# Kernel optimization log

Measured on AMD Instinct MI355X. Metric: run time of the kernel, lower is better.

## Reference

```python
import jax, jax.numpy as jnp
import numpy as np

HEADS = 8
MODEL_DIM = 64
EPS = 1e-5


def _layernorm(x, gamma, beta):
    mu = jnp.mean(x, axis=-1, keepdims=True)
    var = jnp.var(x, axis=-1, keepdims=True)
    return (x - mu) * jax.lax.rsqrt(var + EPS) * gamma + beta


def setup_inputs() -> dict:
    key = jax.random.key(0)
    ks = jax.random.split(key, 5)
    bs, h, w, in_dim = 8, 32, 32, 512
    hd = HEADS * MODEL_DIM  # 512
    s = 0.02
    return {
        "x": jax.random.normal(ks[0], (bs, h, w, in_dim), jnp.float32),
        "Wq": jax.random.normal(ks[1], (in_dim, hd), jnp.float32) * s,
        "Wk": jax.random.normal(ks[2], (in_dim, hd), jnp.float32) * s,
        "Wv": jax.random.normal(ks[3], (in_dim, hd), jnp.float32) * s,
        "Wo": jax.random.normal(ks[4], (hd, in_dim), jnp.float32) * s,
        "gamma": jnp.ones((in_dim,), jnp.float32),
        "beta": jnp.zeros((in_dim,), jnp.float32),
    }


def reference(x, Wq, Wk, Wv, Wo, gamma, beta):
    bs, h, w, in_dim = x.shape
    # pre_norm=True: normalize first; residual uses the normalized x (as in original)
    xn = _layernorm(x, gamma, beta)
    Q = (xn @ Wq).reshape(bs, h, w, HEADS, MODEL_DIM)
    K = (xn @ Wk).reshape(bs, h, w, HEADS, MODEL_DIM)
    V = (xn @ Wv).reshape(bs, h, w, HEADS, MODEL_DIM)
    # full (h,w) x (h,w) correlation per head
    corr = jnp.einsum('bijhd,bklhd->bijhkl', Q, K) / jnp.sqrt(
        jnp.asarray(MODEL_DIM, x.dtype))
    cshape = corr.shape
    attn = jax.nn.softmax(corr.reshape(*cshape[:-2], -1), axis=-1).reshape(cshape)
    logits = jnp.einsum('bijhkl,bklhd->bijhd', attn, V).reshape(bs, h, w, -1)
    out = logits @ Wo + xn
    return out, attn
```

## Files before the change

### kernel.cpp

```cpp
#include <hip/hip_runtime.h>
#include <hip/hip_bf16.h>

typedef __attribute__((ext_vector_type(8))) short bf16x8;
typedef __attribute__((ext_vector_type(4))) short s16x4;
typedef __attribute__((ext_vector_type(4))) float f32x4;

#define DIM 512
#define NH 8
#define HD 64
#define SEQ 1024
#define NB 8
#define ROWS (NB*SEQ)

__device__ __forceinline__ short f2bf(float f) {
  union { float f; unsigned u; } v; v.f = f;
  unsigned r = v.u + 0x7fffu + ((v.u >> 16) & 1u);
  return (short)(r >> 16);
}
__device__ __forceinline__ float bf2f(short s) {
  union { unsigned u; float f; } v; v.u = ((unsigned)(unsigned short)s) << 16;
  return v.f;
}
__device__ __forceinline__ f32x4 mfma16(bf16x8 a, bf16x8 b, f32x4 c) {
  return __builtin_amdgcn_mfma_f32_16x16x32_bf16(a, b, c, 0, 0, 0);
}
__device__ __forceinline__ void gload16(const void* g, void* l) {
  __builtin_amdgcn_global_load_lds(
      (const __attribute__((address_space(1))) unsigned int*)g,
      (__attribute__((address_space(3))) unsigned int*)l, 16, 0, 0);
}
__device__ __forceinline__ void lds_barrier() {
  __builtin_amdgcn_sched_barrier(0);
  asm volatile("s_waitcnt lgkmcnt(0)" ::: "memory");
  __builtin_amdgcn_s_barrier();
  __builtin_amdgcn_sched_barrier(0);
}

__global__ __launch_bounds__(256) void prep_kernel(
    const float* __restrict__ x, const float* __restrict__ gamma,
    const float* __restrict__ beta, short* __restrict__ xnb,
    const float* __restrict__ Wq, const float* __restrict__ Wk,
    const float* __restrict__ Wv, const float* __restrict__ Wo,
    short* __restrict__ WqkvT, short* __restrict__ WoT) {
  __shared__ float tl[64 * 65];
  const int t = threadIdx.x;
  if (blockIdx.x < 2048) {
    const int row = blockIdx.x * 4 + (t >> 6);
    const int lane = t & 63;
    const float4* xr = reinterpret_cast<const float4*>(x + (size_t)row * DIM);
    const float4 a = xr[lane * 2], b2 = xr[lane * 2 + 1];
    float s = a.x + a.y + a.z + a.w + b2.x + b2.y + b2.z + b2.w;
    float sq = a.x*a.x + a.y*a.y + a.z*a.z + a.w*a.w +
               b2.x*b2.x + b2.y*b2.y + b2.z*b2.z + b2.w*b2.w;
    for (int off = 1; off < 64; off <<= 1) {
      s += __shfl_xor(s, off);
      sq += __shfl_xor(sq, off);
    }
    const float mean = s * (1.0f / DIM);
    const float var = sq * (1.0f / DIM) - mean * mean;
    const float rs = rsqrtf(var + 1e-5f);
    const float4 ga = reinterpret_cast<const float4*>(gamma)[lane * 2];
    const float4 gb = reinterpret_cast<const float4*>(gamma)[lane * 2 + 1];
    const float4 ba = reinterpret_cast<const float4*>(beta)[lane * 2];
    const float4 bb = reinterpret_cast<const float4*>(beta)[lane * 2 + 1];
    union { bf16x8 v; short sh[8]; } o;
    o.sh[0] = f2bf((a.x - mean) * rs * ga.x + ba.x);
    o.sh[1] = f2bf((a.y - mean) * rs * ga.y + ba.y);
    o.sh[2] = f2bf((a.z - mean) * rs * ga.z + ba.z);
    o.sh[3] = f2bf((a.w - mean) * rs * ga.w + ba.w);
    o.sh[4] = f2bf((b2.x - mean) * rs * gb.x + bb.x);
    o.sh[5] = f2bf((b2.y - mean) * rs * gb.y + bb.y);
    o.sh[6] = f2bf((b2.z - mean) * rs * gb.z + bb.z);
    o.sh[7] = f2bf((b2.w - mean) * rs * gb.w + bb.w);
    *reinterpret_cast<bf16x8*>(xnb + (size_t)row * DIM + lane * 8) = o.v;
  } else {
    const int bb = blockIdx.x - 2048;
    const int y = bb >> 6;
    const float* W = (y == 0) ? Wq : (y == 1) ? Wk : (y == 2) ? Wv : Wo;
    const int tile = bb & 63;
    const int k0 = (tile >> 3) * 64, n0 = (tile & 7) * 64;
#pragma unroll
    for (int i = 0; i < 16; ++i) {
      const int idx = i * 256 + t;
      const int k = idx >> 6, n = idx & 63;
      tl[n * 65 + k] = W[(size_t)(k0 + k) * 512 + n0 + n];
    }
    __syncthreads();
#pragma unroll
    for (int i = 0; i < 16; ++i) {
      const int idx = i * 256 + t;
      const int n = idx >> 6, k = idx & 63;
      const short v = f2bf(tl[n * 65 + k]);
      if (y < 3) WqkvT[(size_t)(y * 512 + n0 + n) * 512 + k0 + k] = v;
      else       WoT[(size_t)(n0 + n) * 512 + k0 + k] = v;
    }
  }
}

#define GEMM64_MAIN(A_, BT_, m0_, n0_)                                        \
  f32x4 acc[4][4] = {};                                                       \
  {                                                                           \
    const int srow = 8 * w + (lane >> 3);                                     \
    const int sseg = lane & 7;                                                \
    for (int kb = 0; kb < 512; kb += 64) {                                    \
      __syncthreads();                                                        \
      _Pragma("unroll")                                                       \
      for (int p = 0; p < 4; ++p) {                                           \
        const int r = 32 * p + srow;                                          \
        const int gs = 8 * (sseg ^ (r & 7));                                  \
        gload16(A_ + (size_t)(m0_ + r) * 512 + kb + gs,                       \
                &As[(32 * p + 8 * w) * 64]);                                  \
        gload16(BT_ + (size_t)(n0_ + r) * 512 + kb + gs,                      \
                &Bs[(32 * p + 8 * w) * 64]);                                  \
      }                                                                       \
      __syncthreads();                                                        \
      _Pragma("unroll")                                                       \
      for (int half = 0; half < 2; ++half) {                                  \
        bf16x8 af[4], bfr[4];                                                 \
        _Pragma("unroll")                                                     \
        for (int i = 0; i < 4; ++i) {                                         \
          const int ra = 64 * wr + 16 * i + c16;                              \
          af[i] = *reinterpret_cast<const bf16x8*>(                           \
              &As[ra * 64 + 8 * ((4 * half + g) ^ (ra & 7))]);                \
          const int rb = 64 * wc + 16 * i + c16;                              \
          bfr[i] = *reinterpret_cast<const bf16x8*>(                          \
              &Bs[rb * 64 + 8 * ((4 * half + g) ^ (rb & 7))]);                \
        }                                                                     \
        _Pragma("unroll")                                                     \
        for (int i = 0; i < 4; ++i)                                           \
          _Pragma("unroll")                                                   \
          for (int j = 0; j < 4; ++j)                                         \
            acc[i][j] = mfma16(af[i], bfr[j], acc[i][j]);                     \
      }                                                                       \
    }                                                                         \
  }

__global__ __launch_bounds__(256) void gemm_qkv(const short* __restrict__ A,
    const short* __restrict__ BT, short* __restrict__ Qo,
    short* __restrict__ Ko, short* __restrict__ VtF) {
  __shared__ short As[128 * 64];
  __shared__ short Bs[128 * 64];
  const int m0 = blockIdx.x * 128, n0 = blockIdx.y * 128;
  const int t = threadIdx.x, w = t >> 6, lane = t & 63, g = lane >> 4, c16 = lane & 15;
  const int wr = w >> 1, wc = w & 1;
  GEMM64_MAIN(A, BT, m0, n0)
  const int z = n0 >> 9;
  const int nl = n0 & 511;
  if (z < 2) {
    short* O = (z == 0) ? Qo : Ko;
#pragma unroll
    for (int i = 0; i < 4; ++i)
#pragma unroll
      for (int j = 0; j < 4; ++j) {
        const int row0 = m0 + 64 * wr + 16 * i + 4 * g;
        const int col = nl + 64 * wc + 16 * j + c16;
#pragma unroll
        for (int e = 0; e < 4; ++e)
          O[(size_t)(row0 + e) * 512 + col] = f2bf(acc[i][j][e]);
      }
  } else {
#pragma unroll
    for (int i = 0; i < 4; ++i)
#pragma unroll
      for (int j = 0; j < 4; ++j) {
        const int row0 = m0 + 64 * wr + 16 * i + 4 * g;
        const int col = nl + 64 * wc + 16 * j + c16;
        const int bb = row0 >> 10, ss0 = row0 & 1023, hh = col >> 6, dd = col & 63;
        const int cch = ss0 >> 7, kk = ss0 & 127;
        const int w2 = kk >> 5;
        const int g2 = (kk >> 2) & 3;
        const int ee0 = 4 * ((kk >> 4) & 1) + (kk & 3);
        const int dt2 = dd >> 4, c162 = dd & 15;
        s16x4 pv;
#pragma unroll
        for (int e = 0; e < 4; ++e) pv[e] = f2bf(acc[i][j][e]);
        *reinterpret_cast<s16x4*>(
            &VtF[((size_t)((((bb * NH + hh) * 8 + cch) * 4 + w2) * 4 + dt2) << 9) +
                 (g2 * 16 + c162) * 8 + ee0]) = pv;
      }
  }
}

__global__ __launch_bounds__(256) void gemm_out(const short* __restrict__ A,
    const short* __restrict__ BT, const short* __restrict__ xnb,
    float* __restrict__ out) {
  __shared__ short As[128 * 64];
  __shared__ short Bs[128 * 64];
  const int m0 = blockIdx.x * 128, n0 = blockIdx.y * 128;
  const int t = threadIdx.x, w = t >> 6, lane = t & 63, g = lane >> 4, c16 = lane & 15;
  const int wr = w >> 1, wc = w & 1;
  GEMM64_MAIN(A, BT, m0, n0)
#pragma unroll
  for (int i = 0; i < 4; ++i)
#pragma unroll
    for (int j = 0; j < 4; ++j)
#pragma unroll
      for (int e = 0; e < 4; ++e) {
        const int row = m0 + 64 * wr + 16 * i + 4 * g + e;
        const int col = n0 + 64 * wc + 16 * j + c16;
        const size_t idx = (size_t)row * 512 + col;
        out[idx] = acc[i][j][e] + bf2f(xnb[idx]);
      }
}

__global__ __launch_bounds__(256, 2) void attn_kernel(
    const short* __restrict__ Qb, const short* __restrict__ Kb,
    const short* __restrict__ VtF, float* __restrict__ attnOut,
    short* __restrict__ Lg) {
  const int bid = blockIdx.x;
  const int rb = (bid >> 3) & 31;
  const int inst = (bid & 7) * 8 + (bid >> 8);
  const int b = inst >> 3, h = inst & 7;
  const int t = threadIdx.x;
  const int w = t >> 6, lane = t & 63, g = lane >> 4, c16 = lane & 15;
  const int rl = lane >> 3, sgl = lane & 7;

  __shared__ __align__(16) char smem[49664];
  __shared__ float red[2][4][16];
  short* Klds = (short*)smem;
  float* P32a = (float*)(smem + 32768);
  float* P32b = (float*)(smem + 41216);

  const short* qpa = Qb + ((size_t)(b * SEQ + rb * 32 + c16)) * DIM + h * HD + 8 * g;
  const bf16x8 qa0 = *reinterpret_cast<const bf16x8*>(qpa);
  const bf16x8 qa1 = *reinterpret_cast<const bf16x8*>(qpa + 32);
  const bf16x8 qB0 = *reinterpret_cast<const bf16x8*>(qpa + 16 * DIM);
  const bf16x8 qB1 = *reinterpret_cast<const bf16x8*>(qpa + 16 * DIM + 32);

  const short* kgbase = Kb + ((size_t)b * SEQ) * DIM + h * HD;
  const int swz = 8 * (sgl ^ rl);
  const int sw = c16 & 7;

#define KSTAGE(c_, buf_)                                                       \
  do {                                                                         \
    __builtin_amdgcn_sched_barrier(0);                                         \
    _Pragma("unroll") for (int i_ = 0; i_ < 4; ++i_) {                         \
      gload16(kgbase + (size_t)((c_) * 128 + 32 * w + 8 * i_ + rl) * DIM + swz,\
              &Klds[(buf_) * 8192 + (32 * w + 8 * i_) * 64]);                  \
    }                                                                          \
  } while (0)

  KSTAGE(0, 0);
  f32x4 acc[16] = {};
#pragma unroll
  for (int c = 0; c < 8; ++c) {
    if (c < 7) KSTAGE(c + 1, (c + 1) & 1);
    if (c < 7) { asm volatile("s_waitcnt vmcnt(4)" ::: "memory"); }
    else       { asm volatile("s_waitcnt vmcnt(0)" ::: "memory"); }
    __builtin_amdgcn_sched_barrier(0);
    const short* kl = &Klds[(c & 1) * 8192];
#pragma unroll
    for (int j = 0; j < 2; ++j) {
      const int lr = 32 * w + 16 * j + c16;
      bf16x8 k0 = *reinterpret_cast<const bf16x8*>(&kl[lr * 64 + 8 * (g ^ sw)]);
      bf16x8 k1 = *reinterpret_cast<const bf16x8*>(&kl[lr * 64 + 8 * ((g + 4) ^ sw)]);
      const int tt = c * 2 + j;
      acc[tt] = mfma16(k0, qa0, acc[tt]);
      acc[tt] = mfma16(k1, qa1, acc[tt]);
    }
  }

  const short* vf = VtF + (size_t)inst * 65536;
  bf16x8 vreg[4];
#pragma unroll
  for (int dt = 0; dt < 4; ++dt)
    vreg[dt] = *reinterpret_cast<const bf16x8*>(vf + (size_t)((w * 4 + dt) * 512) + lane * 8);
  bf16x8 kreg[4];
#pragma unroll
  for (int i = 0; i < 4; ++i)
    kreg[i] = *reinterpret_cast<const bf16x8*>(
        kgbase + (size_t)(32 * w + 8 * i + rl) * DIM + 8 * sgl);

  float m = -1e30f;
#pragma unroll
  for (int tt = 0; tt < 16; ++tt)
#pragma unroll
    for (int e = 0; e < 4; ++e) {
      acc[tt][e] *= 0.125f;
      m = fmaxf(m, acc[tt][e]);
    }
  m = fmaxf(m, __shfl_xor(m, 16));
  m = fmaxf(m, __shfl_xor(m, 32));
  if (g == 0) red[0][w][c16] = m;
  lds_barrier();
  m = fmaxf(fmaxf(red[0][0][c16], red[0][1][c16]),
            fmaxf(red[0][2][c16], red[0][3][c16]));
  float sm = 0.f;
#pragma unroll
  for (int tt = 0; tt < 16; ++tt)
#pragma unroll
    for (int e = 0; e < 4; ++e) {
      const float p = __expf(acc[tt][e] - m);
      acc[tt][e] = p;
      sm += p;
    }
  sm += __shfl_xor(sm, 16);
  sm += __shfl_xor(sm, 32);
  if (g == 0) red[1][w][c16] = sm;
  lds_barrier();
  const float rinvA = 1.0f / (red[1][0][c16] + red[1][1][c16] +
                              red[1][2][c16] + red[1][3][c16]);

  bf16x8 pA[8];
#pragma unroll
  for (int c = 0; c < 8; ++c) {
    union { bf16x8 v; short sh[8]; } u;
#pragma unroll
    for (int j = 0; j < 2; ++j)
#pragma unroll
      for (int e = 0; e < 4; ++e)
        u.sh[4 * j + e] = f2bf(acc[2 * c + j][e] * rinvA);
    pA[c] = u.v;
  }
#pragma unroll
  for (int tt = 0; tt < 16; ++tt)
#pragma unroll
    for (int e = 0; e < 4; ++e) acc[tt][e] = 0.f;

  f32x4 paccA[4] = {};
  const int qrow = t >> 4, qs = t & 15;
  float* astore = attnOut + (size_t)b * 8388608 +
                  (size_t)(rb * 32 + qrow) * 8192 + h * 1024;
#pragma unroll
  for (int c = 0; c < 8; ++c) {
    lds_barrier();
#pragma unroll
    for (int i = 0; i < 4; ++i)
      *reinterpret_cast<bf16x8*>(
          &Klds[(c & 1) * 8192 + (32 * w + 8 * i + rl) * 64 + 8 * (sgl ^ rl)]) = kreg[i];
    {
      float* P32w = (c & 1) ? P32b : P32a;
      union { bf16x8 v; short sh[8]; } u; u.v = pA[c];
      f32x4 v0, v1;
#pragma unroll
      for (int e = 0; e < 4; ++e) { v0[e] = bf2f(u.sh[e]); v1[e] = bf2f(u.sh[4 + e]); }
      *reinterpret_cast<f32x4*>(&P32w[c16 * 132 + 32 * w + 4 * g]) = v0;
      *reinterpret_cast<f32x4*>(&P32w[c16 * 132 + 32 * w + 16 + 4 * g]) = v1;
    }
    if (c < 7) {
#pragma unroll
      for (int i = 0; i < 4; ++i)
        kreg[i] = *reinterpret_cast<const bf16x8*>(
            kgbase + (size_t)((c + 1) * 128 + 32 * w + 8 * i + rl) * DIM + 8 * sgl);
    }
    lds_barrier();
    {
      const float* P32r = (c & 1) ? P32b : P32a;
      const f32x4 s0 = *reinterpret_cast<const f32x4*>(&P32r[qrow * 132 + 4 * qs]);
      const f32x4 s1 = *reinterpret_cast<const f32x4*>(&P32r[qrow * 132 + 64 + 4 * qs]);
      *reinterpret_cast<f32x4*>(astore + c * 128 + 4 * qs) = s0;
      *reinterpret_cast<f32x4*>(astore + c * 128 + 64 + 4 * qs) = s1;
    }
    const short* kl = &Klds[(c & 1) * 8192];
#pragma unroll
    for (int j = 0; j < 2; ++j) {
      const int lr = 32 * w + 16 * j + c16;
      bf16x8 k0 = *reinterpret_cast<const bf16x8*>(&kl[lr * 64 + 8 * (g ^ sw)]);
      bf16x8 k1 = *reinterpret_cast<const bf16x8*>(&kl[lr * 64 + 8 * ((g + 4) ^ sw)]);
      const int tt = c * 2 + j;
      acc[tt] = mfma16(k0, qB0, acc[tt]);
      acc[tt] = mfma16(k1, qB1, acc[tt]);
    }
#pragma unroll
    for (int dt = 0; dt < 4; ++dt)
      paccA[dt] = mfma16(pA[c], vreg[dt], paccA[dt]);
    if (c < 7) {
#pragma unroll
      for (int dt = 0; dt < 4; ++dt)
        vreg[dt] = *reinterpret_cast<const bf16x8*>(
            vf + (size_t)((((c + 1) * 4 + w) * 4 + dt) * 512) + lane * 8);
    }
  }

#pragma unroll
  for (int dt = 0; dt < 4; ++dt)
    vreg[dt] = *reinterpret_cast<const bf16x8*>(vf + (size_t)((w * 4 + dt) * 512) + lane * 8);

  float mB = -1e30f;
#pragma unroll
  for (int tt = 0; tt < 16; ++tt)
#pragma unroll
    for (int e = 0; e < 4; ++e) {
      acc[tt][e] *= 0.125f;
      mB = fmaxf(mB, acc[tt][e]);
    }
  mB = fmaxf(mB, __shfl_xor(mB, 16));
  mB = fmaxf(mB, __shfl_xor(mB, 32));
  if (g == 0) red[0][w][c16] = mB;
  lds_barrier();
  mB = fmaxf(fmaxf(red[0][0][c16], red[0][1][c16]),
             fmaxf(red[0][2][c16], red[0][3][c16]));
  float smB = 0.f;
#pragma unroll
  for (int tt = 0; tt < 16; ++tt)
#pragma unroll
    for (int e = 0; e < 4; ++e) {
      const float p = __expf(acc[tt][e] - mB);
      acc[tt][e] = p;
      smB += p;
    }
  smB += __shfl_xor(smB, 16);
  smB += __shfl_xor(smB, 32);
  if (g == 0) red[1][w][c16] = smB;
  lds_barrier();
  const float rinvB = 1.0f / (red[1][0][c16] + red[1][1][c16] +
                              red[1][2][c16] + red[1][3][c16]);
  bf16x8 pB[8];
#pragma unroll
  for (int c = 0; c < 8; ++c) {
    union { bf16x8 v; short sh[8]; } u;
#pragma unroll
    for (int j = 0; j < 2; ++j)
#pragma unroll
      for (int e = 0; e < 4; ++e)
        u.sh[4 * j + e] = f2bf(acc[2 * c + j][e] * rinvB);
    pB[c] = u.v;
  }

  f32x4 paccB[4] = {};
  float* astoreB = astore + 16 * 8192;
#pragma unroll
  for (int c = 0; c < 8; ++c) {
    lds_barrier();
    {
      float* P32w = (c & 1) ? P32b : P32a;
      union { bf16x8 v; short sh[8]; } u; u.v = pB[c];
      f32x4 v0, v1;
#pragma unroll
      for (int e = 0; e < 4; ++e) { v0[e] = bf2f(u.sh[e]); v1[e] = bf2f(u.sh[4 + e]); }
      *reinterpret_cast<f32x4*>(&P32w[c16 * 132 + 32 * w + 4 * g]) = v0;
      *reinterpret_cast<f32x4*>(&P32w[c16 * 132 + 32 * w + 16 + 4 * g]) = v1;
    }
    lds_barrier();
    {
      const float* P32r = (c & 1) ? P32b : P32a;
      const f32x4 s0 = *reinterpret_cast<const f32x4*>(&P32r[qrow * 132 + 4 * qs]);
      const f32x4 s1 = *reinterpret_cast<const f32x4*>(&P32r[qrow * 132 + 64 + 4 * qs]);
      *reinterpret_cast<f32x4*>(astoreB + c * 128 + 4 * qs) = s0;
      *reinterpret_cast<f32x4*>(astoreB + c * 128 + 64 + 4 * qs) = s1;
    }
#pragma unroll
    for (int dt = 0; dt < 4; ++dt)
      paccB[dt] = mfma16(pB[c], vreg[dt], paccB[dt]);
    if (c < 7) {
#pragma unroll
      for (int dt = 0; dt < 4; ++dt)
        vreg[dt] = *reinterpret_cast<const bf16x8*>(
            vf + (size_t)((((c + 1) * 4 + w) * 4 + dt) * 512) + lane * 8);
    }
  }

  lds_barrier();
  f32x4* red2 = reinterpret_cast<f32x4*>(smem);
#pragma unroll
  for (int dt = 0; dt < 4; ++dt) red2[(w * 4 + dt) * 64 + lane] = paccA[dt];
  lds_barrier();
  {
    const int dt = w;
    f32x4 s = red2[dt * 64 + lane];
#pragma unroll
    for (int w2 = 1; w2 < 4; ++w2) {
      f32x4 o = red2[(w2 * 4 + dt) * 64 + lane];
#pragma unroll
      for (int e = 0; e < 4; ++e) s[e] += o[e];
    }
    short* lrow = Lg + ((size_t)(b * SEQ + rb * 32 + 4 * g)) * DIM + h * HD + 16 * dt + c16;
#pragma unroll
    for (int e = 0; e < 4; ++e) lrow[(size_t)e * DIM] = f2bf(s[e]);
  }
  lds_barrier();
#pragma unroll
  for (int dt = 0; dt < 4; ++dt) red2[(w * 4 + dt) * 64 + lane] = paccB[dt];
  lds_barrier();
  {
    const int dt = w;
    f32x4 s = red2[dt * 64 + lane];
#pragma unroll
    for (int w2 = 1; w2 < 4; ++w2) {
      f32x4 o = red2[(w2 * 4 + dt) * 64 + lane];
#pragma unroll
      for (int e = 0; e < 4; ++e) s[e] += o[e];
    }
    short* lrow = Lg + ((size_t)(b * SEQ + rb * 32 + 16 + 4 * g)) * DIM + h * HD + 16 * dt + c16;
#pragma unroll
    for (int e = 0; e < 4; ++e) lrow[(size_t)e * DIM] = f2bf(s[e]);
  }
}

extern "C" void kernel_launch(void* const* d_in, const int* in_sizes, int n_in,
                              void* d_out, int out_size, void* d_ws, size_t ws_size,
                              hipStream_t stream) {
  const float* x = (const float*)d_in[0];
  const float* Wq = (const float*)d_in[1];
  const float* Wk = (const float*)d_in[2];
  const float* Wv = (const float*)d_in[3];
  const float* Wo = (const float*)d_in[4];
  const float* gamma = (const float*)d_in[5];
  const float* beta = (const float*)d_in[6];
  float* out = (float*)d_out;
  float* attn = out + (size_t)ROWS * DIM;

  char* ws = (char*)d_ws;
  short* xnb = (short*)ws;
  short* WqkvT = (short*)(ws + (size_t)8 * 1024 * 1024);
  short* WoT = WqkvT + 1536 * 512;
  short* Qb = (short*)(ws + (size_t)10 * 1024 * 1024);
  short* Kbp = (short*)(ws + (size_t)18 * 1024 * 1024);
  short* VtF = (short*)(ws + (size_t)26 * 1024 * 1024);
  short* Lg = (short*)(ws + (size_t)34 * 1024 * 1024);

  prep_kernel<<<2304, 256, 0, stream>>>(x, gamma, beta, xnb, Wq, Wk, Wv, Wo, WqkvT, WoT);
  gemm_qkv<<<dim3(64, 12), 256, 0, stream>>>(xnb, WqkvT, Qb, Kbp, VtF);
  attn_kernel<<<2048, 256, 0, stream>>>(Qb, Kbp, VtF, attn, Lg);
  gemm_out<<<dim3(64, 4), 256, 0, stream>>>(Lg, WoT, xnb, out);
}
```

Measured before the change: 128.4 us.

## Process 64 query rows per block with a rolling software pipeline over four tiles

Each attention block now handles four 16-row query tiles instead of two. It halves the grid and overlaps the QK^T MFMA of the next tile with the attention store and PV MFMA of the current tile in a steady-state loop. K and V are reloaded cyclically across tiles, and each tile's output reduction is folded into the softmax barriers. Attention-probability stores become nontemporal. This is meant to amortise K/V staging and overlap compute with the large attn write, at the cost of fewer blocks (lower parallelism and occupancy slack) and more complex barrier use.

```diff
diff --git a/kernel.cpp b/kernel.cpp
--- a/kernel.cpp
+++ b/kernel.cpp
@@ -208,12 +208,15 @@
     const short* __restrict__ VtF, float* __restrict__ attnOut,
     short* __restrict__ Lg) {
   const int bid = blockIdx.x;
-  const int rb = (bid >> 3) & 31;
-  const int inst = (bid & 7) * 8 + (bid >> 8);
+  const int rb = (bid >> 3) & 15;
+  const int inst = (bid & 7) * 8 + (bid >> 7);
   const int b = inst >> 3, h = inst & 7;
   const int t = threadIdx.x;
   const int w = t >> 6, lane = t & 63, g = lane >> 4, c16 = lane & 15;
   const int rl = lane >> 3, sgl = lane & 7;
+  const int sw = c16 & 7;
+  const int rbase = rb * 64;
+  const int qrow = t >> 4, qs = t & 15;
 
   __shared__ __align__(16) char smem[49664];
   __shared__ float red[2][4][16];
@@ -221,15 +224,9 @@
   float* P32a = (float*)(smem + 32768);
   float* P32b = (float*)(smem + 41216);
 
-  const short* qpa = Qb + ((size_t)(b * SEQ + rb * 32 + c16)) * DIM + h * HD + 8 * g;
-  const bf16x8 qa0 = *reinterpret_cast<const bf16x8*>(qpa);
-  const bf16x8 qa1 = *reinterpret_cast<const bf16x8*>(qpa + 32);
-  const bf16x8 qB0 = *reinterpret_cast<const bf16x8*>(qpa + 16 * DIM);
-  const bf16x8 qB1 = *reinterpret_cast<const bf16x8*>(qpa + 16 * DIM + 32);
-
   const short* kgbase = Kb + ((size_t)b * SEQ) * DIM + h * HD;
+  const short* vf = VtF + (size_t)inst * 65536;
   const int swz = 8 * (sgl ^ rl);
-  const int sw = c16 & 7;
 
 #define KSTAGE(c_, buf_)                                                       \
   do {                                                                         \
@@ -240,250 +237,235 @@
     }                                                                          \
   } while (0)
 
-  KSTAGE(0, 0);
   f32x4 acc[16] = {};
-#pragma unroll
-  for (int c = 0; c < 8; ++c) {
-    if (c < 7) KSTAGE(c + 1, (c + 1) & 1);
-    if (c < 7) { asm volatile("s_waitcnt vmcnt(4)" ::: "memory"); }
-    else       { asm volatile("s_waitcnt vmcnt(0)" ::: "memory"); }
-    __builtin_amdgcn_sched_barrier(0);
-    const short* kl = &Klds[(c & 1) * 8192];
-#pragma unroll
-    for (int j = 0; j < 2; ++j) {
-      const int lr = 32 * w + 16 * j + c16;
-      bf16x8 k0 = *reinterpret_cast<const bf16x8*>(&kl[lr * 64 + 8 * (g ^ sw)]);
-      bf16x8 k1 = *reinterpret_cast<const bf16x8*>(&kl[lr * 64 + 8 * ((g + 4) ^ sw)]);
-      const int tt = c * 2 + j;
-      acc[tt] = mfma16(k0, qa0, acc[tt]);
-      acc[tt] = mfma16(k1, qa1, acc[tt]);
-    }
-  }
-
-  const short* vf = VtF + (size_t)inst * 65536;
-  bf16x8 vreg[4];
-#pragma unroll
-  for (int dt = 0; dt < 4; ++dt)
-    vreg[dt] = *reinterpret_cast<const bf16x8*>(vf + (size_t)((w * 4 + dt) * 512) + lane * 8);
-  bf16x8 kreg[4];
+  {
+    const short* qp = Qb + ((size_t)(b * SEQ + rbase + c16)) * DIM + h * HD + 8 * g;
+    const bf16x8 q0 = *reinterpret_cast<const bf16x8*>(qp);
+    const bf16x8 q1 = *reinterpret_cast<const bf16x8*>(qp + 32);
+    KSTAGE(0, 0);
+#pragma unroll
+    for (int c = 0; c < 8; ++c) {
+      if (c < 7) KSTAGE(c + 1, (c + 1) & 1);
+      if (c < 7) { asm volatile("s_waitcnt vmcnt(4)" ::: "memory"); }
+      else       { asm volatile("s_waitcnt vmcnt(0)" ::: "memory"); }
+      __builtin_amdgcn_sched_barrier(0);
+      const short* kl = &Klds[(c & 1) * 8192];
+#pragma unroll
+      for (int j = 0; j < 2; ++j) {
+        const int lr = 32 * w + 16 * j + c16;
+        bf16x8 k0 = *reinterpret_cast<const bf16x8*>(&kl[lr * 64 + 8 * (g ^ sw)]);
+        bf16x8 k1 = *reinterpret_cast<const bf16x8*>(&kl[lr * 64 + 8 * ((g + 4) ^ sw)]);
+        const int tt = c * 2 + j;
+        acc[tt] = mfma16(k0, q0, acc[tt]);
+        acc[tt] = mfma16(k1, q1, acc[tt]);
+      }
+    }
+  }
+
+  bf16x8 kreg[4], vreg[4];
 #pragma unroll
   for (int i = 0; i < 4; ++i)
     kreg[i] = *reinterpret_cast<const bf16x8*>(
         kgbase + (size_t)(32 * w + 8 * i + rl) * DIM + 8 * sgl);
-
-  float m = -1e30f;
-#pragma unroll
-  for (int tt = 0; tt < 16; ++tt)
-#pragma unroll
-    for (int e = 0; e < 4; ++e) {
-      acc[tt][e] *= 0.125f;
-      m = fmaxf(m, acc[tt][e]);
-    }
-  m = fmaxf(m, __shfl_xor(m, 16));
-  m = fmaxf(m, __shfl_xor(m, 32));
-  if (g == 0) red[0][w][c16] = m;
-  lds_barrier();
-  m = fmaxf(fmaxf(red[0][0][c16], red[0][1][c16]),
-            fmaxf(red[0][2][c16], red[0][3][c16]));
-  float sm = 0.f;
-#pragma unroll
-  for (int tt = 0; tt < 16; ++tt)
-#pragma unroll
-    for (int e = 0; e < 4; ++e) {
-      const float p = __expf(acc[tt][e] - m);
-      acc[tt][e] = p;
-      sm += p;
-    }
-  sm += __shfl_xor(sm, 16);
-  sm += __shfl_xor(sm, 32);
-  if (g == 0) red[1][w][c16] = sm;
-  lds_barrier();
-  const float rinvA = 1.0f / (red[1][0][c16] + red[1][1][c16] +
-                              red[1][2][c16] + red[1][3][c16]);
-
-  bf16x8 pA[8];
-#pragma unroll
-  for (int c = 0; c < 8; ++c) {
-    union { bf16x8 v; short sh[8]; } u;
-#pragma unroll
-    for (int j = 0; j < 2; ++j)
-#pragma unroll
-      for (int e = 0; e < 4; ++e)
-        u.sh[4 * j + e] = f2bf(acc[2 * c + j][e] * rinvA);
-    pA[c] = u.v;
-  }
-#pragma unroll
-  for (int tt = 0; tt < 16; ++tt)
-#pragma unroll
-    for (int e = 0; e < 4; ++e) acc[tt][e] = 0.f;
-
-  f32x4 paccA[4] = {};
-  const int qrow = t >> 4, qs = t & 15;
-  float* astore = attnOut + (size_t)b * 8388608 +
-                  (size_t)(rb * 32 + qrow) * 8192 + h * 1024;
-#pragma unroll
-  for (int c = 0; c < 8; ++c) {
-    lds_barrier();
-#pragma unroll
-    for (int i = 0; i < 4; ++i)
-      *reinterpret_cast<bf16x8*>(
-          &Klds[(c & 1) * 8192 + (32 * w + 8 * i + rl) * 64 + 8 * (sgl ^ rl)]) = kreg[i];
-    {
-      float* P32w = (c & 1) ? P32b : P32a;
-      union { bf16x8 v; short sh[8]; } u; u.v = pA[c];
-      f32x4 v0, v1;
-#pragma unroll
-      for (int e = 0; e < 4; ++e) { v0[e] = bf2f(u.sh[e]); v1[e] = bf2f(u.sh[4 + e]); }
-      *reinterpret_cast<f32x4*>(&P32w[c16 * 132 + 32 * w + 4 * g]) = v0;
-      *reinterpret_cast<f32x4*>(&P32w[c16 * 132 + 32 * w + 16 + 4 * g]) = v1;
-    }
-    if (c < 7) {
-#pragma unroll
-      for (int i = 0; i < 4; ++i)
-        kreg[i] = *reinterpret_cast<const bf16x8*>(
-            kgbase + (size_t)((c + 1) * 128 + 32 * w + 8 * i + rl) * DIM + 8 * sgl);
-    }
-    lds_barrier();
-    {
-      const float* P32r = (c & 1) ? P32b : P32a;
-      const f32x4 s0 = *reinterpret_cast<const f32x4*>(&P32r[qrow * 132 + 4 * qs]);
-      const f32x4 s1 = *reinterpret_cast<const f32x4*>(&P32r[qrow * 132 + 64 + 4 * qs]);
-      *reinterpret_cast<f32x4*>(astore + c * 128 + 4 * qs) = s0;
-      *reinterpret_cast<f32x4*>(astore + c * 128 + 64 + 4 * qs) = s1;
-    }
-    const short* kl = &Klds[(c & 1) * 8192];
-#pragma unroll
-    for (int j = 0; j < 2; ++j) {
-      const int lr = 32 * w + 16 * j + c16;
-      bf16x8 k0 = *reinterpret_cast<const bf16x8*>(&kl[lr * 64 + 8 * (g ^ sw)]);
-      bf16x8 k1 = *reinterpret_cast<const bf16x8*>(&kl[lr * 64 + 8 * ((g + 4) ^ sw)]);
-      const int tt = c * 2 + j;
-      acc[tt] = mfma16(k0, qB0, acc[tt]);
-      acc[tt] = mfma16(k1, qB1, acc[tt]);
-    }
-#pragma unroll
-    for (int dt = 0; dt < 4; ++dt)
-      paccA[dt] = mfma16(pA[c], vreg[dt], paccA[dt]);
-    if (c < 7) {
-#pragma unroll
-      for (int dt = 0; dt < 4; ++dt)
-        vreg[dt] = *reinterpret_cast<const bf16x8*>(
-            vf + (size_t)((((c + 1) * 4 + w) * 4 + dt) * 512) + lane * 8);
-    }
-  }
-
 #pragma unroll
   for (int dt = 0; dt < 4; ++dt)
     vreg[dt] = *reinterpret_cast<const bf16x8*>(vf + (size_t)((w * 4 + dt) * 512) + lane * 8);
 
-  float mB = -1e30f;
-#pragma unroll
-  for (int tt = 0; tt < 16; ++tt)
-#pragma unroll
-    for (int e = 0; e < 4; ++e) {
-      acc[tt][e] *= 0.125f;
-      mB = fmaxf(mB, acc[tt][e]);
-    }
-  mB = fmaxf(mB, __shfl_xor(mB, 16));
-  mB = fmaxf(mB, __shfl_xor(mB, 32));
-  if (g == 0) red[0][w][c16] = mB;
-  lds_barrier();
-  mB = fmaxf(fmaxf(red[0][0][c16], red[0][1][c16]),
-             fmaxf(red[0][2][c16], red[0][3][c16]));
-  float smB = 0.f;
-#pragma unroll
-  for (int tt = 0; tt < 16; ++tt)
-#pragma unroll
-    for (int e = 0; e < 4; ++e) {
-      const float p = __expf(acc[tt][e] - mB);
-      acc[tt][e] = p;
-      smB += p;
-    }
-  smB += __shfl_xor(smB, 16);
-  smB += __shfl_xor(smB, 32);
-  if (g == 0) red[1][w][c16] = smB;
-  lds_barrier();
-  const float rinvB = 1.0f / (red[1][0][c16] + red[1][1][c16] +
-                              red[1][2][c16] + red[1][3][c16]);
-  bf16x8 pB[8];
-#pragma unroll
-  for (int c = 0; c < 8; ++c) {
-    union { bf16x8 v; short sh[8]; } u;
-#pragma unroll
-    for (int j = 0; j < 2; ++j)
-#pragma unroll
-      for (int e = 0; e < 4; ++e)
-        u.sh[4 * j + e] = f2bf(acc[2 * c + j][e] * rinvB);
-    pB[c] = u.v;
-  }
-
-  f32x4 paccB[4] = {};
-  float* astoreB = astore + 16 * 8192;
-#pragma unroll
-  for (int c = 0; c < 8; ++c) {
+  bf16x8 pA[8];
+  {
+    float m = -1e30f;
+#pragma unroll
+    for (int tt = 0; tt < 16; ++tt)
+#pragma unroll
+      for (int e = 0; e < 4; ++e) {
+        acc[tt][e] *= 0.125f;
+        m = fmaxf(m, acc[tt][e]);
+      }
+    m = fmaxf(m, __shfl_xor(m, 16));
+    m = fmaxf(m, __shfl_xor(m, 32));
+    if (g == 0) red[0][w][c16] = m;
     lds_barrier();
-    {
-      float* P32w = (c & 1) ? P32b : P32a;
-      union { bf16x8 v; short sh[8]; } u; u.v = pB[c];
-      f32x4 v0, v1;
-#pragma unroll
-      for (int e = 0; e < 4; ++e) { v0[e] = bf2f(u.sh[e]); v1[e] = bf2f(u.sh[4 + e]); }
-      *reinterpret_cast<f32x4*>(&P32w[c16 * 132 + 32 * w + 4 * g]) = v0;
-      *reinterpret_cast<f32x4*>(&P32w[c16 * 132 + 32 * w + 16 + 4 * g]) = v1;
-    }
+    m = fmaxf(fmaxf(red[0][0][c16], red[0][1][c16]),
+              fmaxf(red[0][2][c16], red[0][3][c16]));
+    float sm = 0.f;
+#pragma unroll
+    for (int tt = 0; tt < 16; ++tt)
+#pragma unroll
+      for (int e = 0; e < 4; ++e) {
+        const float p = __expf(acc[tt][e] - m);
+        acc[tt][e] = p;
+        sm += p;
+      }
+    sm += __shfl_xor(sm, 16);
+    sm += __shfl_xor(sm, 32);
+    if (g == 0) red[1][w][c16] = sm;
     lds_barrier();
-    {
-      const float* P32r = (c & 1) ? P32b : P32a;
-      const f32x4 s0 = *reinterpret_cast<const f32x4*>(&P32r[qrow * 132 + 4 * qs]);
-      const f32x4 s1 = *reinterpret_cast<const f32x4*>(&P32r[qrow * 132 + 64 + 4 * qs]);
-      *reinterpret_cast<f32x4*>(astoreB + c * 128 + 4 * qs) = s0;
-      *reinterpret_cast<f32x4*>(astoreB + c * 128 + 64 + 4 * qs) = s1;
-    }
-#pragma unroll
-    for (int dt = 0; dt < 4; ++dt)
-      paccB[dt] = mfma16(pB[c], vreg[dt], paccB[dt]);
-    if (c < 7) {
+    const float rinv = 1.0f / (red[1][0][c16] + red[1][1][c16] +
+                               red[1][2][c16] + red[1][3][c16]);
+#pragma unroll
+    for (int c = 0; c < 8; ++c) {
+      union { bf16x8 v; short sh[8]; } u;
+#pragma unroll
+      for (int j = 0; j < 2; ++j)
+#pragma unroll
+        for (int e = 0; e < 4; ++e) {
+          u.sh[4 * j + e] = f2bf(acc[2 * c + j][e] * rinv);
+          acc[2 * c + j][e] = 0.f;
+        }
+      pA[c] = u.v;
+    }
+  }
+
+  f32x4 pacc[4] = {};
+  f32x4* red2 = reinterpret_cast<f32x4*>(smem + 32768);
+
+#pragma unroll
+  for (int tau = 0; tau < 4; ++tau) {
+    const bool qk = (tau < 3);
+    bf16x8 qn0, qn1;
+    if (qk) {
+      const short* qn = Qb + ((size_t)(b * SEQ + rbase + (tau + 1) * 16 + c16)) * DIM +
+                        h * HD + 8 * g;
+      qn0 = *reinterpret_cast<const bf16x8*>(qn);
+      qn1 = *reinterpret_cast<const bf16x8*>(qn + 32);
+    }
+    float* astore = attnOut + (size_t)b * 8388608 +
+                    (size_t)(rbase + tau * 16 + qrow) * 8192 + h * 1024;
+#pragma unroll
+    for (int c = 0; c < 8; ++c) {
+      lds_barrier();
+      if (qk) {
+#pragma unroll
+        for (int i = 0; i < 4; ++i)
+          *reinterpret_cast<bf16x8*>(
+              &Klds[(c & 1) * 8192 + (32 * w + 8 * i + rl) * 64 + 8 * (sgl ^ rl)]) = kreg[i];
+      }
+      {
+        float* P32w = (c & 1) ? P32b : P32a;
+        union { bf16x8 v; short sh[8]; } u; u.v = pA[c];
+        f32x4 v0, v1;
+#pragma unroll
+        for (int e = 0; e < 4; ++e) { v0[e] = bf2f(u.sh[e]); v1[e] = bf2f(u.sh[4 + e]); }
+        *reinterpret_cast<f32x4*>(&P32w[c16 * 132 + 32 * w + 4 * g]) = v0;
+        *reinterpret_cast<f32x4*>(&P32w[c16 * 132 + 32 * w + 16 + 4 * g]) = v1;
+      }
+      if (qk) {
+#pragma unroll
+        for (int i = 0; i < 4; ++i)
+          kreg[i] = *reinterpret_cast<const bf16x8*>(
+              kgbase + (size_t)((((c + 1) & 7)) * 128 + 32 * w + 8 * i + rl) * DIM + 8 * sgl);
+      }
+      lds_barrier();
+      {
+        const float* P32r = (c & 1) ? P32b : P32a;
+        const f32x4 s0 = *reinterpret_cast<const f32x4*>(&P32r[qrow * 132 + 4 * qs]);
+        const f32x4 s1 = *reinterpret_cast<const f32x4*>(&P32r[qrow * 132 + 64 + 4 * qs]);
+        __builtin_nontemporal_store(s0, reinterpret_cast<f32x4*>(astore + c * 128 + 4 * qs));
+        __builtin_nontemporal_store(s1, reinterpret_cast<f32x4*>(astore + c * 128 + 64 + 4 * qs));
+      }
+      if (qk) {
+        const short* kl = &Klds[(c & 1) * 8192];
+#pragma unroll
+        for (int j = 0; j < 2; ++j) {
+          const int lr = 32 * w + 16 * j + c16;
+          bf16x8 k0 = *reinterpret_cast<const bf16x8*>(&kl[lr * 64 + 8 * (g ^ sw)]);
+          bf16x8 k1 = *reinterpret_cast<const bf16x8*>(&kl[lr * 64 + 8 * ((g + 4) ^ sw)]);
+          const int tt = c * 2 + j;
+          acc[tt] = mfma16(k0, qn0, acc[tt]);
+          acc[tt] = mfma16(k1, qn1, acc[tt]);
+        }
+      }
 #pragma unroll
       for (int dt = 0; dt < 4; ++dt)
-        vreg[dt] = *reinterpret_cast<const bf16x8*>(
-            vf + (size_t)((((c + 1) * 4 + w) * 4 + dt) * 512) + lane * 8);
-    }
-  }
-
-  lds_barrier();
-  f32x4* red2 = reinterpret_cast<f32x4*>(smem);
-#pragma unroll
-  for (int dt = 0; dt < 4; ++dt) red2[(w * 4 + dt) * 64 + lane] = paccA[dt];
-  lds_barrier();
-  {
-    const int dt = w;
-    f32x4 s = red2[dt * 64 + lane];
-#pragma unroll
-    for (int w2 = 1; w2 < 4; ++w2) {
-      f32x4 o = red2[(w2 * 4 + dt) * 64 + lane];
-#pragma unroll
-      for (int e = 0; e < 4; ++e) s[e] += o[e];
-    }
-    short* lrow = Lg + ((size_t)(b * SEQ + rb * 32 + 4 * g)) * DIM + h * HD + 16 * dt + c16;
-#pragma unroll
-    for (int e = 0; e < 4; ++e) lrow[(size_t)e * DIM] = f2bf(s[e]);
-  }
-  lds_barrier();
-#pragma unroll
-  for (int dt = 0; dt < 4; ++dt) red2[(w * 4 + dt) * 64 + lane] = paccB[dt];
-  lds_barrier();
-  {
-    const int dt = w;
-    f32x4 s = red2[dt * 64 + lane];
-#pragma unroll
-    for (int w2 = 1; w2 < 4; ++w2) {
-      f32x4 o = red2[(w2 * 4 + dt) * 64 + lane];
-#pragma unroll
-      for (int e = 0; e < 4; ++e) s[e] += o[e];
-    }
-    short* lrow = Lg + ((size_t)(b * SEQ + rb * 32 + 16 + 4 * g)) * DIM + h * HD + 16 * dt + c16;
-#pragma unroll
-    for (int e = 0; e < 4; ++e) lrow[(size_t)e * DIM] = f2bf(s[e]);
+        pacc[dt] = mfma16(pA[c], vreg[dt], pacc[dt]);
+      if (!(tau == 3 && c == 7)) {
+#pragma unroll
+        for (int dt = 0; dt < 4; ++dt)
+          vreg[dt] = *reinterpret_cast<const bf16x8*>(
+              vf + (size_t)(((((c + 1) & 7) * 4 + w) * 4 + dt) * 512) + lane * 8);
+      }
+    }
+
+    if (qk) {
+      float m = -1e30f;
+#pragma unroll
+      for (int tt = 0; tt < 16; ++tt)
+#pragma unroll
+        for (int e = 0; e < 4; ++e) {
+          acc[tt][e] *= 0.125f;
+          m = fmaxf(m, acc[tt][e]);
+        }
+      m = fmaxf(m, __shfl_xor(m, 16));
+      m = fmaxf(m, __shfl_xor(m, 32));
+      if (g == 0) red[0][w][c16] = m;
+      lds_barrier();
+#pragma unroll
+      for (int dt = 0; dt < 4; ++dt) red2[(w * 4 + dt) * 64 + lane] = pacc[dt];
+#pragma unroll
+      for (int dt = 0; dt < 4; ++dt)
+#pragma unroll
+        for (int e = 0; e < 4; ++e) pacc[dt][e] = 0.f;
+      m = fmaxf(fmaxf(red[0][0][c16], red[0][1][c16]),
+                fmaxf(red[0][2][c16], red[0][3][c16]));
+      float sm = 0.f;
+#pragma unroll
+      for (int tt = 0; tt < 16; ++tt)
+#pragma unroll
+        for (int e = 0; e < 4; ++e) {
+          const float pe = __expf(acc[tt][e] - m);
+          acc[tt][e] = pe;
+          sm += pe;
+        }
+      sm += __shfl_xor(sm, 16);
+      sm += __shfl_xor(sm, 32);
+      if (g == 0) red[1][w][c16] = sm;
+      lds_barrier();
+      {
+        const int dt = w;
+        f32x4 s = red2[dt * 64 + lane];
+#pragma unroll
+        for (int w2 = 1; w2 < 4; ++w2) {
+          f32x4 o = red2[(w2 * 4 + dt) * 64 + lane];
+#pragma unroll
+          for (int e = 0; e < 4; ++e) s[e] += o[e];
+        }
+        short* lrow = Lg + ((size_t)(b * SEQ + rbase + tau * 16 + 4 * g)) * DIM +
+                      h * HD + 16 * dt + c16;
+#pragma unroll
+        for (int e = 0; e < 4; ++e) lrow[(size_t)e * DIM] = f2bf(s[e]);
+      }
+      const float rinv = 1.0f / (red[1][0][c16] + red[1][1][c16] +
+                                 red[1][2][c16] + red[1][3][c16]);
+#pragma unroll
+      for (int c = 0; c < 8; ++c) {
+        union { bf16x8 v; short sh[8]; } u;
+#pragma unroll
+        for (int j = 0; j < 2; ++j)
+#pragma unroll
+          for (int e = 0; e < 4; ++e) {
+            u.sh[4 * j + e] = f2bf(acc[2 * c + j][e] * rinv);
+            acc[2 * c + j][e] = 0.f;
+          }
+        pA[c] = u.v;
+      }
+    } else {
+      lds_barrier();
+#pragma unroll
+      for (int dt = 0; dt < 4; ++dt) red2[(w * 4 + dt) * 64 + lane] = pacc[dt];
+      lds_barrier();
+      const int dt = w;
+      f32x4 s = red2[dt * 64 + lane];
+#pragma unroll
+      for (int w2 = 1; w2 < 4; ++w2) {
+        f32x4 o = red2[(w2 * 4 + dt) * 64 + lane];
+#pragma unroll
+        for (int e = 0; e < 4; ++e) s[e] += o[e];
+      }
+      short* lrow = Lg + ((size_t)(b * SEQ + rbase + 48 + 4 * g)) * DIM +
+                    h * HD + 16 * dt + c16;
+#pragma unroll
+      for (int e = 0; e < 4; ++e) lrow[(size_t)e * DIM] = f2bf(s[e]);
+    }
   }
 }
 
@@ -511,6 +493,6 @@
 
   prep_kernel<<<2304, 256, 0, stream>>>(x, gamma, beta, xnb, Wq, Wk, Wv, Wo, WqkvT, WoT);
   gemm_qkv<<<dim3(64, 12), 256, 0, stream>>>(xnb, WqkvT, Qb, Kbp, VtF);
-  attn_kernel<<<2048, 256, 0, stream>>>(Qb, Kbp, VtF, attn, Lg);
+  attn_kernel<<<1024, 256, 0, stream>>>(Qb, Kbp, VtF, attn, Lg);
   gemm_out<<<dim3(64, 4), 256, 0, stream>>>(Lg, WoT, xnb, out);
 }
```

New measurement: 144.1 us. +12.3%, slower.
